# Kernel optimization log

Hardware: AMD Instinct MI355X
Metric: run time of the kernel (lower is better)

## Reference

```python
import jax, jax.numpy as jnp
import numpy as np

N = 8192
NFEAT = 784
NUM_CLASSES = 10


def _glorot(key, shape):
    lim = 1.0 / np.sqrt(shape[0])
    return jax.random.uniform(key, shape, jnp.float32, -lim, lim)


def setup_inputs() -> dict:
    key = jax.random.key(0)
    ks = jax.random.split(key, 16)
    x = jax.random.normal(ks[0], (N, NFEAT), jnp.float32)
    adj = (jax.random.uniform(ks[1], (N, N)) < 0.02).astype(jnp.float32)
    adj = jnp.maximum(adj, jnp.eye(N, dtype=jnp.float32))
    dims = [(NFEAT, 256), (256, 128), (256, 256), (128, 128), (128, 128),
            (128, 64), (128, 128), (128, 128), (128, 1)]
    names = ['gcn1', 'd11', 'd12', 'gcn2', 'd21', 'd22', 'gcn3', 'd31', 'd32']
    inp = {'x': x, 'adj': adj}
    for i, (nm, (fi, fo)) in enumerate(zip(names, dims)):
        inp['W_' + nm] = _glorot(ks[2 + i], (fi, fo))
        inp['b_' + nm] = jnp.zeros((fo,), jnp.float32)
    inp['W_fc'] = _glorot(ks[11], (128, NUM_CLASSES))
    inp['b_fc'] = jnp.zeros((NUM_CLASSES,), jnp.float32)
    return inp


def _gcn(x, adj, W, b):
    # Kipf GCN layer: adj @ (x @ W) + b
    return adj @ (x @ W) + b


def _normalize_adj(adj):
    # degree[i,i] = 1/nnz(row_i); out = sqrt(D) @ adj @ sqrt(D)
    deg = jnp.sum(adj != 0, axis=1).astype(adj.dtype)  # [N]
    d = jax.lax.rsqrt(deg)                              # 1/sqrt(deg)
    return adj * d[:, None] * d[None, :]


def reference(x, adj,
              W_gcn1, b_gcn1, W_d11, b_d11, W_d12, b_d12,
              W_gcn2, b_gcn2, W_d21, b_d21, W_d22, b_d22,
              W_gcn3, b_gcn3, W_d31, b_d31, W_d32, b_d32,
              W_fc, b_fc):
    adj = _normalize_adj(adj)
    x = _gcn(x, adj, W_gcn1, b_gcn1)                  # [N, 256]
    z1 = _gcn(x, adj, W_d11, b_d11)                   # [N, 128]
    s1 = jax.nn.softmax(_gcn(x, adj, W_d12, b_d12), axis=1)  # [N, 256]
    x = s1.T @ z1                                     # [256, 128]
    adj = s1.T @ adj @ s1                             # [256, 256]
    x = _gcn(x, adj, W_gcn2, b_gcn2)                  # [256, 128]
    z2 = _gcn(x, adj, W_d21, b_d21)                   # [256, 128]
    s2 = jax.nn.softmax(_gcn(x, adj, W_d22, b_d22), axis=1)  # [256, 64]
    x = s2.T @ z2                                     # [64, 128]
    adj = s2.T @ (adj @ s2)                           # [64, 64]
    x = _gcn(x, adj, W_gcn3, b_gcn3)                  # [64, 128]
    z3 = _gcn(x, adj, W_d31, b_d31)                   # [64, 128]
    s3 = jax.nn.softmax(_gcn(x, adj, W_d32, b_d32), axis=1)  # [64, 1]
    x = s3.T @ z3                                     # [1, 128]
    out = x @ W_fc + b_fc                             # [1, 10]
    return jax.nn.log_softmax(out, axis=1)
```

## Files before the change

kernel.cpp:

```cpp
#include <hip/hip_runtime.h>
#include <math.h>

#define NROWS 8192
#define MAXNNZ 512

__global__ void build_csr_kernel(const float* __restrict__ adj, int* __restrict__ cols,
                                 int* __restrict__ cnt, float* __restrict__ dvec) {
    int row = blockIdx.x;
    __shared__ int lcnt;
    if (threadIdx.x == 0) lcnt = 0;
    __syncthreads();
    const float* arow = adj + (size_t)row * NROWS;
    int* crow = cols + (size_t)row * MAXNNZ;
    int tid = threadIdx.x;
#pragma unroll
    for (int j = 0; j < NROWS / 1024; ++j) {
        int c = (j * 256 + tid) * 4;
        float4 v = *reinterpret_cast<const float4*>(&arow[c]);
        if (v.x != 0.0f) { int p = atomicAdd(&lcnt, 1); if (p < MAXNNZ) crow[p] = c; }
        if (v.y != 0.0f) { int p = atomicAdd(&lcnt, 1); if (p < MAXNNZ) crow[p] = c + 1; }
        if (v.z != 0.0f) { int p = atomicAdd(&lcnt, 1); if (p < MAXNNZ) crow[p] = c + 2; }
        if (v.w != 0.0f) { int p = atomicAdd(&lcnt, 1); if (p < MAXNNZ) crow[p] = c + 3; }
    }
    __syncthreads();
    if (threadIdx.x == 0) {
        int n = lcnt; if (n > MAXNNZ) n = MAXNNZ;
        cnt[row] = n;
        dvec[row] = rsqrtf((float)lcnt);
    }
}

__global__ void pack_kernel(const float* __restrict__ Wd11, const float* __restrict__ Wd12,
                            const float* __restrict__ bd11, const float* __restrict__ bd12,
                            const float* __restrict__ Wd21, const float* __restrict__ Wd22,
                            const float* __restrict__ bd21, const float* __restrict__ bd22,
                            float* __restrict__ Wcat1, float* __restrict__ bcat1,
                            float* __restrict__ Wcat2, float* __restrict__ bcat2) {
    int idx = blockIdx.x * 256 + threadIdx.x;
    if (idx < 256 * 384) {
        int r = idx / 384, c = idx % 384;
        Wcat1[idx] = (c < 128) ? Wd11[r * 128 + c] : Wd12[r * 256 + (c - 128)];
        return;
    }
    idx -= 256 * 384;
    if (idx < 128 * 192) {
        int r = idx / 192, c = idx % 192;
        Wcat2[idx] = (c < 128) ? Wd21[r * 128 + c] : Wd22[r * 64 + (c - 128)];
        return;
    }
    idx -= 128 * 192;
    if (idx < 384) { bcat1[idx] = (idx < 128) ? bd11[idx] : bd12[idx - 128]; return; }
    idx -= 384;
    if (idx < 192) { bcat2[idx] = (idx < 128) ? bd21[idx] : bd22[idx - 128]; return; }
}

__global__ void spmm_sliced_kernel(const int* __restrict__ cols, const int* __restrict__ cnt,
                                   const float* __restrict__ dvec, const float* __restrict__ H,
                                   const float* __restrict__ bias, float* __restrict__ out,
                                   int ldh, int ldo) {
    int row = blockIdx.x;
    int cb = blockIdx.y * 128;
    int tid = threadIdx.x;
    __shared__ int sidx[MAXNNZ];
    __shared__ float sw[MAXNNZ];
    int n = cnt[row];
    const int* crow = cols + (size_t)row * MAXNNZ;
    for (int i = tid; i < n; i += 128) {
        int c = crow[i];
        sidx[i] = c * ldh + cb;
        sw[i] = dvec[c];
    }
    __syncthreads();
    float acc = 0.0f;
    int i = 0;
    for (; i + 4 <= n; i += 4) {
        float h0 = H[sidx[i]   + tid];
        float h1 = H[sidx[i+1] + tid];
        float h2 = H[sidx[i+2] + tid];
        float h3 = H[sidx[i+3] + tid];
        acc += sw[i]*h0 + sw[i+1]*h1 + sw[i+2]*h2 + sw[i+3]*h3;
    }
    for (; i < n; i++) acc += sw[i] * H[sidx[i] + tid];
    float r = dvec[row] * acc;
    if (bias) r += bias[cb + tid];
    out[(size_t)row * ldo + cb + tid] = r;
}

__global__ void gemm_bias_kernel(const float* __restrict__ A, const float* __restrict__ B,
                                 const float* __restrict__ bias, float* __restrict__ C,
                                 int M, int N, int K, int lda, int ldb, int ldc) {
    __shared__ float As[16][68];
    __shared__ float Bs[16][68];
    int tx = threadIdx.x, ty = threadIdx.y;
    int tid = ty * 16 + tx;
    int row0 = blockIdx.y * 64, col0 = blockIdx.x * 64;
    int am = tid >> 2, ak = (tid & 3) * 4;
    int bk = tid >> 4, bn = (tid & 15) * 4;
    float acc[4][4] = {};
    for (int k0 = 0; k0 < K; k0 += 16) {
        int gm = row0 + am;
        float4 va = make_float4(0.f, 0.f, 0.f, 0.f);
        if (gm < M) va = *reinterpret_cast<const float4*>(&A[(size_t)gm * lda + k0 + ak]);
        As[ak + 0][am] = va.x; As[ak + 1][am] = va.y;
        As[ak + 2][am] = va.z; As[ak + 3][am] = va.w;
        float4 vb = *reinterpret_cast<const float4*>(&B[(size_t)(k0 + bk) * ldb + col0 + bn]);
        *reinterpret_cast<float4*>(&Bs[bk][bn]) = vb;
        __syncthreads();
#pragma unroll
        for (int k = 0; k < 16; ++k) {
            float4 a = *reinterpret_cast<const float4*>(&As[k][ty * 4]);
            float4 b = *reinterpret_cast<const float4*>(&Bs[k][tx * 4]);
            float av[4] = {a.x, a.y, a.z, a.w};
            float bv[4] = {b.x, b.y, b.z, b.w};
#pragma unroll
            for (int i = 0; i < 4; ++i)
#pragma unroll
                for (int j = 0; j < 4; ++j)
                    acc[i][j] += av[i] * bv[j];
        }
        __syncthreads();
    }
    float4 bb = make_float4(0.f, 0.f, 0.f, 0.f);
    if (bias) bb = *reinterpret_cast<const float4*>(&bias[col0 + tx * 4]);
#pragma unroll
    for (int i = 0; i < 4; ++i) {
        int gm = row0 + ty * 4 + i;
        if (gm >= M) continue;
        float4 v = make_float4(acc[i][0] + bb.x, acc[i][1] + bb.y,
                               acc[i][2] + bb.z, acc[i][3] + bb.w);
        *reinterpret_cast<float4*>(&C[(size_t)gm * ldc + col0 + tx * 4]) = v;
    }
}

__global__ void gemm_atn_kernel(const float* __restrict__ A, const float* __restrict__ B,
                                float* __restrict__ C, int M, int N, int K, int KC,
                                int lda, int ldb, int ldc) {
    __shared__ float As[16][68];
    __shared__ float Bs[16][68];
    int tx = threadIdx.x, ty = threadIdx.y;
    int tid = ty * 16 + tx;
    int row0 = blockIdx.y * 64, col0 = blockIdx.x * 64;
    int kbeg = blockIdx.z * KC;
    int kend = kbeg + KC; if (kend > K) kend = K;
    int ka = tid >> 4, m4 = (tid & 15) * 4;
    int bk = tid >> 4, bn = (tid & 15) * 4;
    float acc[4][4] = {};
    for (int k0 = kbeg; k0 < kend; k0 += 16) {
        int gm = row0 + m4;
        float4 va = make_float4(0.f, 0.f, 0.f, 0.f);
        if (gm < M) va = *reinterpret_cast<const float4*>(&A[(size_t)(k0 + ka) * lda + gm]);
        *reinterpret_cast<float4*>(&As[ka][m4]) = va;
        float4 vb = *reinterpret_cast<const float4*>(&B[(size_t)(k0 + bk) * ldb + col0 + bn]);
        *reinterpret_cast<float4*>(&Bs[bk][bn]) = vb;
        __syncthreads();
#pragma unroll
        for (int k = 0; k < 16; ++k) {
            float4 a = *reinterpret_cast<const float4*>(&As[k][ty * 4]);
            float4 b = *reinterpret_cast<const float4*>(&Bs[k][tx * 4]);
            float av[4] = {a.x, a.y, a.z, a.w};
            float bv[4] = {b.x, b.y, b.z, b.w};
#pragma unroll
            for (int i = 0; i < 4; ++i)
#pragma unroll
                for (int j = 0; j < 4; ++j)
                    acc[i][j] += av[i] * bv[j];
        }
        __syncthreads();
    }
#pragma unroll
    for (int i = 0; i < 4; ++i) {
        int gm = row0 + ty * 4 + i;
        if (gm >= M) continue;
#pragma unroll
        for (int j = 0; j < 4; ++j)
            atomicAdd(&C[(size_t)gm * ldc + col0 + tx * 4 + j], acc[i][j]);
    }
}

__global__ void softmax_rows_kernel(float* __restrict__ data, int NC, int ld, int off) {
    int row = blockIdx.x;
    float* p = data + (size_t)row * ld + off;
    __shared__ float red[256];
    int tid = threadIdx.x;
    float m = -INFINITY;
    for (int c = tid; c < NC; c += 256) m = fmaxf(m, p[c]);
    red[tid] = m; __syncthreads();
    for (int s = 128; s > 0; s >>= 1) {
        if (tid < s) red[tid] = fmaxf(red[tid], red[tid + s]);
        __syncthreads();
    }
    m = red[0]; __syncthreads();
    float sum = 0.0f;
    for (int c = tid; c < NC; c += 256) sum += expf(p[c] - m);
    red[tid] = sum; __syncthreads();
    for (int s = 128; s > 0; s >>= 1) {
        if (tid < s) red[tid] += red[tid + s];
        __syncthreads();
    }
    float inv = 1.0f / red[0];
    for (int c = tid; c < NC; c += 256) p[c] = expf(p[c] - m) * inv;
}

__global__ void final_kernel(const float* __restrict__ z3, const float* __restrict__ Wfc,
                             const float* __restrict__ bfc, float* __restrict__ out) {
    __shared__ float v[128];
    __shared__ float o[10];
    int tid = threadIdx.x;
    float a = 0.0f;
#pragma unroll
    for (int i = 0; i < 64; i++) a += z3[i * 128 + tid];
    v[tid] = a;
    __syncthreads();
    if (tid < 10) {
        float s = 0.0f;
        for (int k = 0; k < 128; k++) s += v[k] * Wfc[k * 10 + tid];
        o[tid] = s + bfc[tid];
    }
    __syncthreads();
    if (tid == 0) {
        float m = -INFINITY;
        for (int c = 0; c < 10; c++) m = fmaxf(m, o[c]);
        float s = 0.0f;
        for (int c = 0; c < 10; c++) s += expf(o[c] - m);
        float lse = m + logf(s);
        for (int c = 0; c < 10; c++) out[c] = o[c] - lse;
    }
}

extern "C" void kernel_launch(void* const* d_in, const int* in_sizes, int n_in,
                              void* d_out, int out_size, void* d_ws, size_t ws_size,
                              hipStream_t stream) {
    const float* x      = (const float*)d_in[0];
    const float* adj    = (const float*)d_in[1];
    const float* W_gcn1 = (const float*)d_in[2];
    const float* b_gcn1 = (const float*)d_in[3];
    const float* W_d11  = (const float*)d_in[4];
    const float* b_d11  = (const float*)d_in[5];
    const float* W_d12  = (const float*)d_in[6];
    const float* b_d12  = (const float*)d_in[7];
    const float* W_gcn2 = (const float*)d_in[8];
    const float* b_gcn2 = (const float*)d_in[9];
    const float* W_d21  = (const float*)d_in[10];
    const float* b_d21  = (const float*)d_in[11];
    const float* W_d22  = (const float*)d_in[12];
    const float* b_d22  = (const float*)d_in[13];
    const float* W_gcn3 = (const float*)d_in[14];
    const float* b_gcn3 = (const float*)d_in[15];
    const float* W_d31  = (const float*)d_in[16];
    const float* b_d31  = (const float*)d_in[17];
    const float* W_fc   = (const float*)d_in[20];
    const float* b_fc   = (const float*)d_in[21];

    char* ws = (char*)d_ws;
    size_t off = 0;
    auto alloc = [&](size_t bytes) -> char* {
        char* p = ws + off;
        off = (off + bytes + 255) & ~(size_t)255;
        return p;
    };
    int*   cols  = (int*)  alloc((size_t)NROWS * MAXNNZ * 4);
    int*   cnt   = (int*)  alloc((size_t)NROWS * 4);
    float* dvec  = (float*)alloc((size_t)NROWS * 4);
    float* XW1   = (float*)alloc((size_t)NROWS * 256 * 4);
    float* x1    = (float*)alloc((size_t)NROWS * 256 * 4);
    float* u1    = (float*)alloc((size_t)NROWS * 256 * 4);
    float* Tcat  = (float*)alloc((size_t)NROWS * 384 * 4);
    float* s1    = (float*)alloc((size_t)NROWS * 256 * 4);
    float* Xp    = (float*)alloc(256 * 128 * 4);
    float* adj2  = (float*)alloc(256 * 256 * 4);
    float* Xp2   = (float*)alloc(64 * 128 * 4);
    float* adj3  = (float*)alloc(64 * 64 * 4);
    size_t zero_bytes = 256*128*4 + 256*256*4 + 64*128*4 + 64*64*4;
    float* XW2   = (float*)alloc(256 * 128 * 4);
    float* x2    = (float*)alloc(256 * 128 * 4);
    float* T2cat = (float*)alloc(256 * 192 * 4);
    float* Z2cat = (float*)alloc(256 * 192 * 4);
    float* AS2   = (float*)alloc(256 * 64 * 4);
    float* T30   = (float*)alloc(64 * 128 * 4);
    float* x3    = (float*)alloc(64 * 128 * 4);
    float* T31   = (float*)alloc(64 * 128 * 4);
    float* z3    = (float*)alloc(64 * 128 * 4);
    float* Wcat1 = (float*)alloc(256 * 384 * 4);
    float* bcat1 = (float*)alloc(384 * 4);
    float* Wcat2 = (float*)alloc(128 * 192 * 4);
    float* bcat2 = (float*)alloc(192 * 4);

    dim3 blk2(16, 16);

    pack_kernel<<<483, 256, 0, stream>>>(W_d11, W_d12, b_d11, b_d12,
                                         W_d21, W_d22, b_d21, b_d22,
                                         Wcat1, bcat1, Wcat2, bcat2);
    hipMemsetAsync(Xp, 0, zero_bytes, stream);
    build_csr_kernel<<<NROWS, 256, 0, stream>>>(adj, cols, cnt, dvec);

    gemm_bias_kernel<<<dim3(4, 128), blk2, 0, stream>>>(x, W_gcn1, nullptr, XW1,
                                                        NROWS, 256, 784, 784, 256, 256);
    spmm_sliced_kernel<<<dim3(NROWS, 2), 128, 0, stream>>>(cols, cnt, dvec, XW1, b_gcn1,
                                                           x1, 256, 256);
    spmm_sliced_kernel<<<dim3(NROWS, 2), 128, 0, stream>>>(cols, cnt, dvec, x1, nullptr,
                                                           u1, 256, 256);
    gemm_bias_kernel<<<dim3(6, 128), blk2, 0, stream>>>(u1, Wcat1, bcat1, Tcat,
                                                        NROWS, 384, 256, 256, 384, 384);
    softmax_rows_kernel<<<NROWS, 256, 0, stream>>>(Tcat, 256, 384, 128);
    spmm_sliced_kernel<<<dim3(NROWS, 2), 128, 0, stream>>>(cols, cnt, dvec, Tcat + 128,
                                                           nullptr, s1, 384, 256);

    gemm_atn_kernel<<<dim3(2, 4, 32), blk2, 0, stream>>>(Tcat + 128, Tcat, Xp,
                                                         256, 128, NROWS, 256, 384, 384, 128);
    gemm_atn_kernel<<<dim3(4, 4, 32), blk2, 0, stream>>>(Tcat + 128, s1, adj2,
                                                         256, 256, NROWS, 256, 384, 256, 256);

    gemm_bias_kernel<<<dim3(2, 4), blk2, 0, stream>>>(Xp, W_gcn2, nullptr, XW2,
                                                      256, 128, 128, 128, 128, 128);
    gemm_bias_kernel<<<dim3(2, 4), blk2, 0, stream>>>(adj2, XW2, b_gcn2, x2,
                                                      256, 128, 256, 256, 128, 128);
    gemm_bias_kernel<<<dim3(3, 4), blk2, 0, stream>>>(x2, Wcat2, nullptr, T2cat,
                                                      256, 192, 128, 128, 192, 192);
    gemm_bias_kernel<<<dim3(3, 4), blk2, 0, stream>>>(adj2, T2cat, bcat2, Z2cat,
                                                      256, 192, 256, 256, 192, 192);
    softmax_rows_kernel<<<256, 256, 0, stream>>>(Z2cat, 64, 192, 128);
    gemm_bias_kernel<<<dim3(1, 4), blk2, 0, stream>>>(adj2, Z2cat + 128, nullptr, AS2,
                                                      256, 64, 256, 256, 192, 64);
    gemm_atn_kernel<<<dim3(2, 1, 1), blk2, 0, stream>>>(Z2cat + 128, Z2cat, Xp2,
                                                        64, 128, 256, 256, 192, 192, 128);
    gemm_atn_kernel<<<dim3(1, 1, 1), blk2, 0, stream>>>(Z2cat + 128, AS2, adj3,
                                                        64, 64, 256, 256, 192, 64, 64);

    gemm_bias_kernel<<<dim3(2, 1), blk2, 0, stream>>>(Xp2, W_gcn3, nullptr, T30,
                                                      64, 128, 128, 128, 128, 128);
    gemm_bias_kernel<<<dim3(2, 1), blk2, 0, stream>>>(adj3, T30, b_gcn3, x3,
                                                      64, 128, 64, 64, 128, 128);
    gemm_bias_kernel<<<dim3(2, 1), blk2, 0, stream>>>(x3, W_d31, nullptr, T31,
                                                      64, 128, 128, 128, 128, 128);
    gemm_bias_kernel<<<dim3(2, 1), blk2, 0, stream>>>(adj3, T31, b_d31, z3,
                                                      64, 128, 64, 64, 128, 128);
    final_kernel<<<1, 128, 0, stream>>>(z3, W_fc, b_fc, (float*)d_out);
}
```

Measured before the change: 926.2 us.

## Switch first-level GEMMs to bf16 MFMA and store SpMM intermediates in bf16

Replaces the fp32 tiled GEMMs for x@W_gcn1 and u1@Wcat1 with a bf16 MFMA kernel using pre-transposed, K-padded weights and a bf16 copy of x. The SpMM intermediates (XW1, x1, u1, softmax s1) are stored in bf16 and processed by a single 256-thread block per row instead of two 128-column slices. The aim is to use matrix cores and halve the memory traffic of the gather-heavy sparse products. The cost is an extra cast pass over x, bf16 rounding error across several chained layers, and reliance on dimensions being multiples of the tile sizes.

```diff
diff --git a/kernel.cpp b/kernel.cpp
--- a/kernel.cpp
+++ b/kernel.cpp
@@ -1,8 +1,15 @@
 #include <hip/hip_runtime.h>
+#include <hip/hip_bf16.h>
 #include <math.h>
 
 #define NROWS 8192
 #define MAXNNZ 512
+
+typedef __attribute__((ext_vector_type(8))) short short8v;
+typedef __attribute__((ext_vector_type(4))) float floatx4;
+
+__device__ inline void storev(float* p, float v) { *p = v; }
+__device__ inline void storev(__hip_bfloat16* p, float v) { *p = __float2bfloat16(v); }
 
 __global__ void build_csr_kernel(const float* __restrict__ adj, int* __restrict__ cols,
                                  int* __restrict__ cnt, float* __restrict__ dvec) {
@@ -30,60 +37,135 @@
     }
 }
 
-__global__ void pack_kernel(const float* __restrict__ Wd11, const float* __restrict__ Wd12,
+__global__ void cast_x_kernel(const float* __restrict__ x, __hip_bfloat16* __restrict__ xb) {
+    int row = blockIdx.x;
+    int tid = threadIdx.x;
+    const float* src = x + (size_t)row * 784;
+    __hip_bfloat16* dst = xb + (size_t)row * 800;
+    for (int c = tid; c < 800; c += 256)
+        dst[c] = (c < 784) ? __float2bfloat16(src[c]) : __float2bfloat16(0.0f);
+}
+
+__global__ void prep_kernel(const float* __restrict__ Wg1,
+                            const float* __restrict__ Wd11, const float* __restrict__ Wd12,
                             const float* __restrict__ bd11, const float* __restrict__ bd12,
                             const float* __restrict__ Wd21, const float* __restrict__ Wd22,
                             const float* __restrict__ bd21, const float* __restrict__ bd22,
-                            float* __restrict__ Wcat1, float* __restrict__ bcat1,
-                            float* __restrict__ Wcat2, float* __restrict__ bcat2) {
+                            __hip_bfloat16* __restrict__ Wg1T, __hip_bfloat16* __restrict__ Wcat1T,
+                            float* __restrict__ bcat1, float* __restrict__ Wcat2,
+                            float* __restrict__ bcat2) {
     int idx = blockIdx.x * 256 + threadIdx.x;
-    if (idx < 256 * 384) {
-        int r = idx / 384, c = idx % 384;
-        Wcat1[idx] = (c < 128) ? Wd11[r * 128 + c] : Wd12[r * 256 + (c - 128)];
+    if (idx < 256 * 800) {
+        int n = idx / 800, k = idx % 800;
+        Wg1T[idx] = __float2bfloat16(k < 784 ? Wg1[k * 256 + n] : 0.0f);
         return;
     }
-    idx -= 256 * 384;
+    idx -= 256 * 800;
+    if (idx < 384 * 256) {
+        int n = idx / 256, k = idx % 256;
+        float v = (n < 128) ? Wd11[k * 128 + n] : Wd12[k * 256 + (n - 128)];
+        Wcat1T[idx] = __float2bfloat16(v);
+        return;
+    }
+    idx -= 384 * 256;
+    if (idx < 384) { bcat1[idx] = (idx < 128) ? bd11[idx] : bd12[idx - 128]; return; }
+    idx -= 384;
     if (idx < 128 * 192) {
         int r = idx / 192, c = idx % 192;
         Wcat2[idx] = (c < 128) ? Wd21[r * 128 + c] : Wd22[r * 64 + (c - 128)];
         return;
     }
     idx -= 128 * 192;
-    if (idx < 384) { bcat1[idx] = (idx < 128) ? bd11[idx] : bd12[idx - 128]; return; }
-    idx -= 384;
     if (idx < 192) { bcat2[idx] = (idx < 128) ? bd21[idx] : bd22[idx - 128]; return; }
 }
 
-__global__ void spmm_sliced_kernel(const int* __restrict__ cols, const int* __restrict__ cnt,
-                                   const float* __restrict__ dvec, const float* __restrict__ H,
-                                   const float* __restrict__ bias, float* __restrict__ out,
-                                   int ldh, int ldo) {
+template<typename OUT>
+__global__ void gemm_mfma_kernel(const __hip_bfloat16* __restrict__ A,
+                                 const __hip_bfloat16* __restrict__ BT,
+                                 const float* __restrict__ bias,
+                                 OUT* __restrict__ C, int K,
+                                 int lda, int ldb, int ldc) {
+    __shared__ __hip_bfloat16 As[128][40];
+    __shared__ __hip_bfloat16 Bs[64][40];
+    int tid = threadIdx.x;
+    int w = tid >> 6, lane = tid & 63;
+    int row0 = blockIdx.y * 128, col0 = blockIdx.x * 64;
+    int lrow = lane & 15, kb = (lane >> 4) * 8;
+    floatx4 acc[2][4] = {};
+    int ar = tid >> 1, akh = (tid & 1) * 16;
+    int bn = tid >> 2, bkh = (tid & 3) * 8;
+    for (int k0 = 0; k0 < K; k0 += 32) {
+        {
+            const float4* src = reinterpret_cast<const float4*>(&A[(size_t)(row0 + ar) * lda + k0 + akh]);
+            float4 v0 = src[0], v1 = src[1];
+            *reinterpret_cast<float4*>(&As[ar][akh]) = v0;
+            *reinterpret_cast<float4*>(&As[ar][akh + 8]) = v1;
+        }
+        {
+            float4 v = *reinterpret_cast<const float4*>(&BT[(size_t)(col0 + bn) * ldb + k0 + bkh]);
+            *reinterpret_cast<float4*>(&Bs[bn][bkh]) = v;
+        }
+        __syncthreads();
+        short8v af[2], bf[4];
+#pragma unroll
+        for (int mi = 0; mi < 2; ++mi)
+            af[mi] = *reinterpret_cast<const short8v*>(&As[w * 32 + mi * 16 + lrow][kb]);
+#pragma unroll
+        for (int ni = 0; ni < 4; ++ni)
+            bf[ni] = *reinterpret_cast<const short8v*>(&Bs[ni * 16 + lrow][kb]);
+#pragma unroll
+        for (int mi = 0; mi < 2; ++mi)
+#pragma unroll
+            for (int ni = 0; ni < 4; ++ni)
+                acc[mi][ni] = __builtin_amdgcn_mfma_f32_16x16x32_bf16(af[mi], bf[ni], acc[mi][ni], 0, 0, 0);
+        __syncthreads();
+    }
+#pragma unroll
+    for (int mi = 0; mi < 2; ++mi) {
+#pragma unroll
+        for (int ni = 0; ni < 4; ++ni) {
+            int gcol = col0 + ni * 16 + (lane & 15);
+            float bb = bias ? bias[gcol] : 0.0f;
+#pragma unroll
+            for (int r = 0; r < 4; ++r) {
+                int grow = row0 + w * 32 + mi * 16 + (lane >> 4) * 4 + r;
+                storev(&C[(size_t)grow * ldc + gcol], acc[mi][ni][r] + bb);
+            }
+        }
+    }
+}
+
+template<typename TOUT>
+__global__ void spmm_bf16_kernel(const int* __restrict__ cols, const int* __restrict__ cnt,
+                                 const float* __restrict__ dvec,
+                                 const __hip_bfloat16* __restrict__ H,
+                                 const float* __restrict__ bias, TOUT* __restrict__ out,
+                                 int ldh, int ldo) {
     int row = blockIdx.x;
-    int cb = blockIdx.y * 128;
     int tid = threadIdx.x;
     __shared__ int sidx[MAXNNZ];
     __shared__ float sw[MAXNNZ];
     int n = cnt[row];
     const int* crow = cols + (size_t)row * MAXNNZ;
-    for (int i = tid; i < n; i += 128) {
+    for (int i = tid; i < n; i += 256) {
         int c = crow[i];
-        sidx[i] = c * ldh + cb;
+        sidx[i] = c * ldh;
         sw[i] = dvec[c];
     }
     __syncthreads();
     float acc = 0.0f;
     int i = 0;
     for (; i + 4 <= n; i += 4) {
-        float h0 = H[sidx[i]   + tid];
-        float h1 = H[sidx[i+1] + tid];
-        float h2 = H[sidx[i+2] + tid];
-        float h3 = H[sidx[i+3] + tid];
+        float h0 = __bfloat162float(H[sidx[i]   + tid]);
+        float h1 = __bfloat162float(H[sidx[i+1] + tid]);
+        float h2 = __bfloat162float(H[sidx[i+2] + tid]);
+        float h3 = __bfloat162float(H[sidx[i+3] + tid]);
         acc += sw[i]*h0 + sw[i+1]*h1 + sw[i+2]*h2 + sw[i+3]*h3;
     }
-    for (; i < n; i++) acc += sw[i] * H[sidx[i] + tid];
+    for (; i < n; i++) acc += sw[i] * __bfloat162float(H[sidx[i] + tid]);
     float r = dvec[row] * acc;
-    if (bias) r += bias[cb + tid];
-    out[(size_t)row * ldo + cb + tid] = r;
+    if (bias) r += bias[tid];
+    storev(&out[(size_t)row * ldo + tid], r);
 }
 
 __global__ void gemm_bias_kernel(const float* __restrict__ A, const float* __restrict__ B,
@@ -177,7 +259,8 @@
     }
 }
 
-__global__ void softmax_rows_kernel(float* __restrict__ data, int NC, int ld, int off) {
+__global__ void softmax_rows_kernel(float* __restrict__ data, int NC, int ld, int off,
+                                    __hip_bfloat16* __restrict__ bout, int ldb) {
     int row = blockIdx.x;
     float* p = data + (size_t)row * ld + off;
     __shared__ float red[256];
@@ -198,7 +281,11 @@
         __syncthreads();
     }
     float inv = 1.0f / red[0];
-    for (int c = tid; c < NC; c += 256) p[c] = expf(p[c] - m) * inv;
+    for (int c = tid; c < NC; c += 256) {
+        float v = expf(p[c] - m) * inv;
+        p[c] = v;
+        if (bout) bout[(size_t)row * ldb + c] = __float2bfloat16(v);
+    }
 }
 
 __global__ void final_kernel(const float* __restrict__ z3, const float* __restrict__ Wfc,
@@ -261,9 +348,13 @@
     int*   cols  = (int*)  alloc((size_t)NROWS * MAXNNZ * 4);
     int*   cnt   = (int*)  alloc((size_t)NROWS * 4);
     float* dvec  = (float*)alloc((size_t)NROWS * 4);
-    float* XW1   = (float*)alloc((size_t)NROWS * 256 * 4);
-    float* x1    = (float*)alloc((size_t)NROWS * 256 * 4);
-    float* u1    = (float*)alloc((size_t)NROWS * 256 * 4);
+    __hip_bfloat16* xb     = (__hip_bfloat16*)alloc((size_t)NROWS * 800 * 2);
+    __hip_bfloat16* Wg1T   = (__hip_bfloat16*)alloc(256 * 800 * 2);
+    __hip_bfloat16* Wcat1T = (__hip_bfloat16*)alloc(384 * 256 * 2);
+    __hip_bfloat16* XW1b   = (__hip_bfloat16*)alloc((size_t)NROWS * 256 * 2);
+    __hip_bfloat16* x1b    = (__hip_bfloat16*)alloc((size_t)NROWS * 256 * 2);
+    __hip_bfloat16* u1b    = (__hip_bfloat16*)alloc((size_t)NROWS * 256 * 2);
+    __hip_bfloat16* ASb    = (__hip_bfloat16*)alloc((size_t)NROWS * 256 * 2);
     float* Tcat  = (float*)alloc((size_t)NROWS * 384 * 4);
     float* s1    = (float*)alloc((size_t)NROWS * 256 * 4);
     float* Xp    = (float*)alloc(256 * 128 * 4);
@@ -280,30 +371,30 @@
     float* x3    = (float*)alloc(64 * 128 * 4);
     float* T31   = (float*)alloc(64 * 128 * 4);
     float* z3    = (float*)alloc(64 * 128 * 4);
-    float* Wcat1 = (float*)alloc(256 * 384 * 4);
+    float* Wcat2 = (float*)alloc(128 * 192 * 4);
     float* bcat1 = (float*)alloc(384 * 4);
-    float* Wcat2 = (float*)alloc(128 * 192 * 4);
     float* bcat2 = (float*)alloc(192 * 4);
 
     dim3 blk2(16, 16);
 
-    pack_kernel<<<483, 256, 0, stream>>>(W_d11, W_d12, b_d11, b_d12,
-                                         W_d21, W_d22, b_d21, b_d22,
-                                         Wcat1, bcat1, Wcat2, bcat2);
+    prep_kernel<<<(256*800 + 384*256 + 384 + 128*192 + 192 + 255) / 256, 256, 0, stream>>>(
+        W_gcn1, W_d11, W_d12, b_d11, b_d12, W_d21, W_d22, b_d21, b_d22,
+        Wg1T, Wcat1T, bcat1, Wcat2, bcat2);
+    cast_x_kernel<<<NROWS, 256, 0, stream>>>(x, xb);
     hipMemsetAsync(Xp, 0, zero_bytes, stream);
     build_csr_kernel<<<NROWS, 256, 0, stream>>>(adj, cols, cnt, dvec);
 
-    gemm_bias_kernel<<<dim3(4, 128), blk2, 0, stream>>>(x, W_gcn1, nullptr, XW1,
-                                                        NROWS, 256, 784, 784, 256, 256);
-    spmm_sliced_kernel<<<dim3(NROWS, 2), 128, 0, stream>>>(cols, cnt, dvec, XW1, b_gcn1,
-                                                           x1, 256, 256);
-    spmm_sliced_kernel<<<dim3(NROWS, 2), 128, 0, stream>>>(cols, cnt, dvec, x1, nullptr,
-                                                           u1, 256, 256);
-    gemm_bias_kernel<<<dim3(6, 128), blk2, 0, stream>>>(u1, Wcat1, bcat1, Tcat,
-                                                        NROWS, 384, 256, 256, 384, 384);
-    softmax_rows_kernel<<<NROWS, 256, 0, stream>>>(Tcat, 256, 384, 128);
-    spmm_sliced_kernel<<<dim3(NROWS, 2), 128, 0, stream>>>(cols, cnt, dvec, Tcat + 128,
-                                                           nullptr, s1, 384, 256);
+    gemm_mfma_kernel<__hip_bfloat16><<<dim3(4, 64), 256, 0, stream>>>(
+        xb, Wg1T, nullptr, XW1b, 800, 800, 800, 256);
+    spmm_bf16_kernel<__hip_bfloat16><<<NROWS, 256, 0, stream>>>(
+        cols, cnt, dvec, XW1b, b_gcn1, x1b, 256, 256);
+    spmm_bf16_kernel<__hip_bfloat16><<<NROWS, 256, 0, stream>>>(
+        cols, cnt, dvec, x1b, nullptr, u1b, 256, 256);
+    gemm_mfma_kernel<float><<<dim3(6, 64), 256, 0, stream>>>(
+        u1b, Wcat1T, bcat1, Tcat, 256, 256, 256, 384);
+    softmax_rows_kernel<<<NROWS, 256, 0, stream>>>(Tcat, 256, 384, 128, ASb, 256);
+    spmm_bf16_kernel<float><<<NROWS, 256, 0, stream>>>(
+        cols, cnt, dvec, ASb, nullptr, s1, 256, 256);
 
     gemm_atn_kernel<<<dim3(2, 4, 32), blk2, 0, stream>>>(Tcat + 128, Tcat, Xp,
                                                          256, 128, NROWS, 256, 384, 384, 128);
@@ -318,7 +409,7 @@
                                                       256, 192, 128, 128, 192, 192);
     gemm_bias_kernel<<<dim3(3, 4), blk2, 0, stream>>>(adj2, T2cat, bcat2, Z2cat,
                                                       256, 192, 256, 256, 192, 192);
-    softmax_rows_kernel<<<256, 256, 0, stream>>>(Z2cat, 64, 192, 128);
+    softmax_rows_kernel<<<256, 256, 0, stream>>>(Z2cat, 64, 192, 128, nullptr, 0);
     gemm_bias_kernel<<<dim3(1, 4), blk2, 0, stream>>>(adj2, Z2cat + 128, nullptr, AS2,
                                                       256, 64, 256, 256, 192, 64);
     gemm_atn_kernel<<<dim3(2, 1, 1), blk2, 0, stream>>>(Z2cat + 128, Z2cat, Xp2,
```

New measurement: 871.5 us. 1.06x faster.
